# Performance work log

Hardware: AMD Instinct MI355X
Metric: run time of the kernel (lower is better)

## Reference

```python
import jax, jax.numpy as jnp
import numpy as np

R, DIL = 3, 2  # radius, dilation for neighbor correlation


def conv2d(x, w, b):
    # standard 3x3 stride-1 SAME conv, NCHW / OIHW
    y = jax.lax.conv_general_dilated(x, w, (1, 1), 'SAME',
                                     dimension_numbers=('NCHW', 'OIHW', 'NCHW'))
    return y + b[None, :, None, None]


def bilinear_gather(x, py, px):
    # x: (n,c,h,w); py/px: (n,K,h,w) float sampling coords; zero outside bounds
    n, c, h, w = x.shape
    y0 = jnp.floor(py); x0 = jnp.floor(px)
    wy = py - y0; wx = px - x0
    xf = x.reshape(n, c, h * w)

    def gather(yi, xi):
        valid = ((yi >= 0) & (yi < h) & (xi >= 0) & (xi < w)).astype(x.dtype)
        yc = jnp.clip(yi, 0, h - 1).astype(jnp.int32)
        xc = jnp.clip(xi, 0, w - 1).astype(jnp.int32)
        idx = (yc * w + xc).reshape(n, -1)  # (n, K*h*w)
        v = jax.vmap(lambda f, i: f[:, i])(xf, idx)  # (n, c, K*h*w)
        return v.reshape(n, c, *yi.shape[1:]) * valid[:, None]

    v00 = gather(y0, x0); v01 = gather(y0, x0 + 1)
    v10 = gather(y0 + 1, x0); v11 = gather(y0 + 1, x0 + 1)
    wy_ = wy[:, None]; wx_ = wx[:, None]
    return (v00 * (1 - wy_) * (1 - wx_) + v01 * (1 - wy_) * wx_
            + v10 * wy_ * (1 - wx_) + v11 * wy_ * wx_)


def dcn(x, w, b, ow, ob):
    # DCNv2-style modulated deformable 3x3 conv, stride 1, pad 1, 1 deformable group.
    # Offset/mask predicted by an internal conv: channels = [dy(9), dx(9), mask(9)].
    n, c, h, w_ = x.shape
    K = 9
    om = conv2d(x, ow, ob)  # (n, 27, h, w)
    dy, dx = om[:, :K], om[:, K:2 * K]
    mask = jax.nn.sigmoid(om[:, 2 * K:])
    ky, kx = jnp.meshgrid(jnp.arange(-1, 2), jnp.arange(-1, 2), indexing='ij')
    ky = ky.reshape(K).astype(x.dtype); kx = kx.reshape(K).astype(x.dtype)
    yy = jnp.arange(h, dtype=x.dtype)[None, None, :, None]
    xx = jnp.arange(w_, dtype=x.dtype)[None, None, None, :]
    py = yy + ky[None, :, None, None] + dy  # (n,K,h,w)
    px = xx + kx[None, :, None, None] + dx
    samp = bilinear_gather(x, py, px) * mask[:, None]  # (n,c,K,h,w)
    return jnp.einsum('nckhw,ock->nohw', samp, w.reshape(w.shape[0], c, K)) + b[None, :, None, None]


def ncf(f1, f2, radius, dilation):
    # neighbor_correlation_filter: unfold-based sliding-window dot-product attention
    n, c, h, w = f2.shape
    k = 2 * radius + 1
    pad = (k - 1) * dilation // 2
    f2p = jnp.pad(f2, ((0, 0), (0, 0), (pad, pad), (pad, pad)))
    # (n,c,K,h,w), tap order (ky outer, kx inner) matching F.unfold row-major layout
    patches = jnp.stack([f2p[:, :, i * dilation:i * dilation + h, j * dilation:j * dilation + w]
                         for i in range(k) for j in range(k)], axis=2)
    corr = jnp.einsum('nchw,nckhw->nkhw', f1, patches) / jnp.sqrt(jnp.asarray(c, f1.dtype))
    attn = jax.nn.softmax(corr, axis=1)
    sample = jnp.einsum('nkhw,nckhw->nchw', attn, patches)
    return sample, corr


def stargru(x, t, zw, zb, zow, zob, hw, hb, how, hob):
    tx = jnp.concatenate([x, t], axis=1)
    z = jax.nn.sigmoid(dcn(tx, zw, zb, zow, zob))
    r, _ = ncf(t, x, R, DIL)
    xt = jnp.tanh(dcn(jnp.concatenate([r, t], axis=1), hw, hb, how, hob))
    return (1.0 - z) * t + z * xt


def setup_inputs():
    key = jax.random.key(0)
    N, CIN, CH, H, W = 2, 256, 64, 96, 96
    ks = iter(jax.random.split(key, 32))

    def rn(shape, s=0.05):
        return jax.random.normal(next(ks), shape, jnp.float32) * s

    inp = {
        'x': jax.random.normal(next(ks), (N, CIN, H, W), jnp.float32),
        'template': jax.random.normal(next(ks), (N, CH, H, W), jnp.float32),
        'w_in': rn((CH, CIN, 3, 3)), 'b_in': jnp.zeros((CH,), jnp.float32),
        'w_out': rn((CIN, CH, 3, 3)), 'b_out': jnp.zeros((CIN,), jnp.float32),
    }
    for pre in ('enh_z', 'enh_h', 'upd_z', 'upd_h'):
        inp[pre + '_w'] = rn((CH, 2 * CH, 3, 3))
        inp[pre + '_b'] = jnp.zeros((CH,), jnp.float32)
        inp[pre + '_ow'] = rn((27, 2 * CH, 3, 3), 0.01)  # offset/mask conv (small init)
        inp[pre + '_ob'] = jnp.zeros((27,), jnp.float32)
    return inp


def reference(x, template, w_in, b_in, w_out, b_out,
              enh_z_w, enh_z_b, enh_z_ow, enh_z_ob,
              enh_h_w, enh_h_b, enh_h_ow, enh_h_ob,
              upd_z_w, upd_z_b, upd_z_ow, upd_z_ob,
              upd_h_w, upd_h_b, upd_h_ow, upd_h_ob):
    # CrossUpdate forward, post-first-frame branch (self.template is not None)
    xh = conv2d(x, w_in, b_in)
    x_enh = stargru(template, xh,
                    enh_z_w, enh_z_b, enh_z_ow, enh_z_ob,
                    enh_h_w, enh_h_b, enh_h_ow, enh_h_ob)
    new_template = stargru(xh, template,
                           upd_z_w, upd_z_b, upd_z_ow, upd_z_ob,
                           upd_h_w, upd_h_b, upd_h_ow, upd_h_ob)
    out = conv2d(x_enh, w_out, b_out)
    return (out, new_template)
```

## Files before the change

kernel.cpp:

```cpp
#include <hip/hip_runtime.h>
#include <hip/hip_bf16.h>

typedef __hip_bfloat16 bf16;
typedef unsigned short u16;
typedef unsigned int u32;
typedef __attribute__((ext_vector_type(8))) short short8;
typedef __attribute__((ext_vector_type(4))) short bh4;
typedef __attribute__((ext_vector_type(4))) float floatx4;

constexpr int N_ = 2, H_ = 96, W_ = 96, HW_ = H_ * W_;
constexpr int CIN_ = 256, CH_ = 64, C2_ = 128;

__device__ __forceinline__ float sigm(float v) { return 1.0f / (1.0f + __expf(-v)); }
__device__ __forceinline__ short f2b(float v) { bf16 h = __float2bfloat16(v); return *reinterpret_cast<short*>(&h); }
__device__ __forceinline__ float b2f(short s) {
    union { u32 i; float f; } v; v.i = ((u32)(u16)s) << 16; return v.f;
}

constexpr int A_IN_OFF = 0,                         A_IN_SZ  = 64 * 2304;
constexpr int A_OUT_OFF = A_IN_OFF + A_IN_SZ,       A_OUT_SZ = 256 * 576;
constexpr int A_OFF_OFF = A_OUT_OFF + A_OUT_SZ,     A_OFF_SZ = 64 * 1152;
constexpr int A_DCN_OFF = A_OFF_OFF + 4 * A_OFF_SZ, A_DCN_SZ = 64 * 1152;
constexpr int A_TOT = A_DCN_OFF + 4 * A_DCN_SZ;

__global__ __launch_bounds__(256) void cvt_weights(
        const float* __restrict__ w_in, const float* __restrict__ w_out,
        const float* __restrict__ ow0, const float* __restrict__ ow1,
        const float* __restrict__ ow2, const float* __restrict__ ow3,
        const float* __restrict__ w0, const float* __restrict__ w1,
        const float* __restrict__ w2, const float* __restrict__ w3,
        u16* __restrict__ dst) {
    int id = blockIdx.x * 256 + threadIdx.x;
    if (id >= A_TOT) return;
    float v;
    if (id < A_OUT_OFF) {
        int l = id; int m = l / 2304, k = l % 2304; int tap = k >> 8, ic = k & 255;
        v = w_in[m * 2304 + ic * 9 + tap];
    } else if (id < A_OFF_OFF) {
        int l = id - A_OUT_OFF; int m = l / 576, k = l % 576; int tap = k / 64, ic = k & 63;
        v = w_out[m * 576 + ic * 9 + tap];
    } else if (id < A_DCN_OFF) {
        int l = id - A_OFF_OFF; int i = l / A_OFF_SZ, l2 = l % A_OFF_SZ;
        int m = l2 / 1152, k = l2 % 1152; int tap = k >> 7, ic = k & 127;
        const float* s = (i == 0) ? ow0 : (i == 1) ? ow1 : (i == 2) ? ow2 : ow3;
        v = (m < 27) ? s[m * 1152 + ic * 9 + tap] : 0.f;
    } else {
        int l = id - A_DCN_OFF; int i = l / A_DCN_SZ, l2 = l % A_DCN_SZ;
        int m = l2 / 1152, k = l2 % 1152; int tap = k >> 7, c = k & 127;
        const float* s = (i == 0) ? w0 : (i == 1) ? w1 : (i == 2) ? w2 : w3;
        v = s[m * 1152 + c * 9 + tap];
    }
    short sb = f2b(v);
    dst[id] = *reinterpret_cast<u16*>(&sb);
}

__global__ __launch_bounds__(256) void to_nhwc(const float* __restrict__ src, u16* __restrict__ dst, int C) {
    int id = blockIdx.x * 256 + threadIdx.x;
    int c8n = C >> 3;
    if (id >= N_ * HW_ * c8n) return;
    int c8 = id % c8n;
    int pix = id / c8n;
    int n = pix / HW_, p = pix % HW_;
    const float* s = src + ((size_t)n * C + c8 * 8) * HW_ + p;
    short8 vv;
#pragma unroll
    for (int j = 0; j < 8; ++j) vv[j] = f2b(s[(size_t)j * HW_]);
    *reinterpret_cast<short8*>(dst + (size_t)pix * C + c8 * 8) = vv;
}

__global__ __launch_bounds__(256) void concat_dual(const float* __restrict__ tpl, const float* __restrict__ xh,
                                                   u16* __restrict__ ta, u16* __restrict__ tb) {
    int id = blockIdx.x * 256 + threadIdx.x;
    if (id >= N_ * HW_ * 16) return;
    int c8 = id & 15;
    int pix = id >> 4;
    int n = pix / HW_, p = pix % HW_;
    int c = c8 * 8;
    const float* s = (c < 64) ? tpl + ((size_t)n * 64 + c) * HW_ + p
                              : xh + ((size_t)n * 64 + (c - 64)) * HW_ + p;
    short8 vv;
#pragma unroll
    for (int j = 0; j < 8; ++j) vv[j] = f2b(s[(size_t)j * HW_]);
    *reinterpret_cast<short8*>(ta + (size_t)pix * 128 + c) = vv;
    *reinterpret_cast<short8*>(tb + (size_t)pix * 128 + ((c + 64) & 127)) = vv;
}

template <int IC, int OCST>
__device__ __forceinline__ void conv_core(const u16* __restrict__ X,
                                          const u16* __restrict__ A,
                                          const float* __restrict__ bias,
                                          float* __restrict__ out,
                                          int r, int mt, int t) {
    constexpr int K = IC * 9;
    constexpr int ICC = IC / 64;
    __shared__ __align__(16) u16 Xl[3][50][72];
    int n = r / 192;
    int rr = r % 192;
    int y = rr >> 1, px0 = (rr & 1) * 48;
    int w = t >> 6, lane = t & 63, lm = lane & 15, q = lane >> 4;
    const u16* Arow = A + (size_t)(mt * 64 + w * 16 + lm) * K + q * 8;
    floatx4 acc[3];
#pragma unroll
    for (int a = 0; a < 3; ++a) acc[a] = {0.f, 0.f, 0.f, 0.f};
    const short8 zz = {0, 0, 0, 0, 0, 0, 0, 0};

    for (int icc = 0; icc < ICC; ++icc) {
        short8 af[9][2];
#pragma unroll
        for (int tap = 0; tap < 9; ++tap)
#pragma unroll
            for (int ks = 0; ks < 2; ++ks)
                af[tap][ks] = *reinterpret_cast<const short8*>(Arow + tap * IC + icc * 64 + ks * 32);
        __syncthreads();
#pragma unroll
        for (int it = 0; it < 5; ++it) {
            int id = it * 256 + t;
            if (id < 1200) {
                int ch8 = id & 7;
                int tmp = id >> 3;
                int pxl = tmp % 50, row = tmp / 50;
                int xg = px0 - 1 + pxl;
                int yg = y - 1 + row;
                bool vld = (yg >= 0) && (yg < 96) && (xg >= 0) && (xg < 96);
                short8 vv = zz;
                if (vld)
                    vv = *reinterpret_cast<const short8*>(
                        X + ((size_t)(n * HW_ + yg * 96 + xg)) * IC + icc * 64 + ch8 * 8);
                *reinterpret_cast<short8*>(&Xl[row][pxl][ch8 * 8]) = vv;
            }
        }
        __syncthreads();
#pragma unroll
        for (int tap = 0; tap < 9; ++tap) {
            int ky = tap / 3, kx = tap % 3;
#pragma unroll
            for (int ks = 0; ks < 2; ++ks) {
#pragma unroll
                for (int nf = 0; nf < 3; ++nf) {
                    short8 bv = *reinterpret_cast<const short8*>(&Xl[ky][nf * 16 + lm + kx][ks * 32 + q * 8]);
                    acc[nf] = __builtin_amdgcn_mfma_f32_16x16x32_bf16(af[tap][ks], bv, acc[nf], 0, 0, 0);
                }
            }
        }
    }
    int ocb = mt * 64 + w * 16 + q * 4;
#pragma unroll
    for (int nf = 0; nf < 3; ++nf) {
        int px = px0 + nf * 16 + lm;
#pragma unroll
        for (int rr2 = 0; rr2 < 4; ++rr2) {
            int oc = ocb + rr2;
            if (oc < OCST)
                out[((size_t)(n * OCST + oc)) * HW_ + y * 96 + px] = acc[nf][rr2] + bias[oc];
        }
    }
}

template <int IC, int OCST>
__global__ __launch_bounds__(256) void conv_gemm(const u16* __restrict__ X,
                                                 const u16* __restrict__ A,
                                                 const float* __restrict__ bias,
                                                 float* __restrict__ out) {
    conv_core<IC, OCST>(X, A, bias, out, blockIdx.x % 384, blockIdx.x / 384, threadIdx.x);
}

__global__ __launch_bounds__(256) void conv_gemm2(const u16* __restrict__ X0, const u16* __restrict__ X1,
                                                  const u16* __restrict__ A0, const u16* __restrict__ A1,
                                                  const float* __restrict__ b0, const float* __restrict__ b1,
                                                  float* __restrict__ o0, float* __restrict__ o1) {
    int inst = blockIdx.x / 384, r = blockIdx.x % 384;
    conv_core<C2_, 27>(inst ? X1 : X0, inst ? A1 : A0, inst ? b1 : b0, inst ? o1 : o0, r, 0, threadIdx.x);
}

__device__ __forceinline__ void dcn_core(const u16* __restrict__ txh,
                                         const float* __restrict__ om,
                                         const u16* __restrict__ A,
                                         const float* __restrict__ bias,
                                         float* __restrict__ out,
                                         int r, int t) {
    __shared__ __align__(16) u16 Bl[48][72];
    __shared__ float s_wy[432], s_wx[432], s_m[432];
    __shared__ int s_y0[432], s_x0[432];
    int n = r / 192;
    int rr = r % 192;
    int y = rr >> 1, px0 = (rr & 1) * 48;
    for (int e = t; e < 432; e += 256) {
        int k9 = e / 48, xl = e % 48;
        int x = px0 + xl;
        const float* ob = om + (size_t)n * 27 * HW_ + y * 96 + x;
        float dy = ob[(size_t)k9 * HW_];
        float dx = ob[(size_t)(9 + k9) * HW_];
        float ml = ob[(size_t)(18 + k9) * HW_];
        float py = (float)y + (float)(k9 / 3 - 1) + dy;
        float px = (float)x + (float)(k9 % 3 - 1) + dx;
        float fy = floorf(py), fx = floorf(px);
        s_y0[e] = (int)fy; s_x0[e] = (int)fx;
        s_wy[e] = py - fy; s_wx[e] = px - fx; s_m[e] = sigm(ml);
    }
    int w = t >> 6, lane = t & 63, lm = lane & 15, q = lane >> 4;
    const u16* Arow = A + (size_t)(w * 16 + lm) * 1152 + q * 8;
    floatx4 acc[3];
#pragma unroll
    for (int a = 0; a < 3; ++a) acc[a] = {0.f, 0.f, 0.f, 0.f};
    const u16* txn = txh + (size_t)n * HW_ * 128;
    const short8 zz = {0, 0, 0, 0, 0, 0, 0, 0};

    for (int kc = 0; kc < 18; ++kc) {
        int tap = kc >> 1, c0 = (kc & 1) * 64;
        short8 af[2];
#pragma unroll
        for (int ks = 0; ks < 2; ++ks)
            af[ks] = *reinterpret_cast<const short8*>(Arow + kc * 64 + ks * 32);
        __syncthreads();
#pragma unroll
        for (int i = 0; i < 2; ++i) {
            int id = i * 256 + t;
            if (id < 384) {
                int px = id >> 3, ch8 = id & 7;
                int ce = tap * 48 + px;
                int y0 = s_y0[ce], x0 = s_x0[ce];
                float wy = s_wy[ce], wx = s_wx[ce], m = s_m[ce];
                float w00 = (1.f - wy) * (1.f - wx) * m;
                float w01 = (1.f - wy) * wx * m;
                float w10 = wy * (1.f - wx) * m;
                float w11 = wy * wx * m;
                bool yv0 = (y0 >= 0) & (y0 < 96), yv1 = (y0 >= -1) & (y0 < 95);
                bool xv0 = (x0 >= 0) & (x0 < 96), xv1 = (x0 >= -1) & (x0 < 95);
                const u16* base = txn + (long)(y0 * 96 + x0) * 128 + c0 + ch8 * 8;
                short8 v00 = (yv0 && xv0) ? *reinterpret_cast<const short8*>(base) : zz;
                short8 v01 = (yv0 && xv1) ? *reinterpret_cast<const short8*>(base + 128) : zz;
                short8 v10 = (yv1 && xv0) ? *reinterpret_cast<const short8*>(base + 96 * 128) : zz;
                short8 v11 = (yv1 && xv1) ? *reinterpret_cast<const short8*>(base + 96 * 128 + 128) : zz;
                short8 vv;
#pragma unroll
                for (int j = 0; j < 8; ++j) {
                    float f = b2f(v00[j]) * w00 + b2f(v01[j]) * w01 +
                              b2f(v10[j]) * w10 + b2f(v11[j]) * w11;
                    vv[j] = f2b(f);
                }
                *reinterpret_cast<short8*>(&Bl[px][ch8 * 8]) = vv;
            }
        }
        __syncthreads();
#pragma unroll
        for (int ks = 0; ks < 2; ++ks)
#pragma unroll
            for (int nf = 0; nf < 3; ++nf) {
                short8 bv = *reinterpret_cast<const short8*>(&Bl[nf * 16 + lm][ks * 32 + q * 8]);
                acc[nf] = __builtin_amdgcn_mfma_f32_16x16x32_bf16(af[ks], bv, acc[nf], 0, 0, 0);
            }
    }
    int ocb = w * 16 + q * 4;
#pragma unroll
    for (int nf = 0; nf < 3; ++nf) {
        int px = px0 + nf * 16 + lm;
#pragma unroll
        for (int rr2 = 0; rr2 < 4; ++rr2) {
            int oc = ocb + rr2;
            out[((size_t)(n * CH_ + oc)) * HW_ + y * 96 + px] = acc[nf][rr2] + bias[oc];
        }
    }
}

__global__ __launch_bounds__(256) void dcn_gemm2(const u16* __restrict__ X0, const u16* __restrict__ X1,
                                                 const float* __restrict__ om0, const float* __restrict__ om1,
                                                 const u16* __restrict__ A0, const u16* __restrict__ A1,
                                                 const float* __restrict__ b0, const float* __restrict__ b1,
                                                 float* __restrict__ o0, float* __restrict__ o1) {
    int inst = blockIdx.x / 384, r = blockIdx.x % 384;
    dcn_core(inst ? X1 : X0, inst ? om1 : om0, inst ? A1 : A0, inst ? b1 : b0, inst ? o1 : o0, r, threadIdx.x);
}

__global__ __launch_bounds__(256, 4) void ncf2(const u16* __restrict__ in0, const u16* __restrict__ in1,
                                               u16* __restrict__ out0, u16* __restrict__ out1) {
    __shared__ float sc[16][52];
    int t = threadIdx.x;
    int inst = blockIdx.x / 1152, bb = blockIdx.x % 1152;
    const u16* txh = inst ? in1 : in0;
    u16* txh2 = inst ? out1 : out0;
    int lp = t >> 4, j = t & 15;
    int gpx = bb * 16 + lp;
    int n = gpx / HW_, p = gpx % HW_;
    int y = p / 96, x = p % 96;
    const u16* base = txh + (size_t)n * HW_ * 128;
    const u16* f1p = base + (size_t)p * 128 + 64;

    float f1f[64];
#pragma unroll
    for (int c8 = 0; c8 < 8; ++c8) {
        short8 a = *reinterpret_cast<const short8*>(f1p + c8 * 8);
#pragma unroll
        for (int u = 0; u < 8; ++u) f1f[c8 * 8 + u] = b2f(a[u]);
    }
    for (int k = j; k < 49; k += 16) {
        int yy = y + (k / 7) * 2 - 6, xx = x + (k % 7) * 2 - 6;
        float s = 0.f;
        if (yy >= 0 && yy < 96 && xx >= 0 && xx < 96) {
            const u16* f2p = base + (size_t)(yy * 96 + xx) * 128;
#pragma unroll
            for (int c8 = 0; c8 < 8; ++c8) {
                short8 b = *reinterpret_cast<const short8*>(f2p + c8 * 8);
#pragma unroll
                for (int u = 0; u < 8; ++u) s += f1f[c8 * 8 + u] * b2f(b[u]);
            }
        }
        sc[lp][k] = s * 0.125f;
    }
    float mx = -1e30f;
    for (int k = j; k < 49; k += 16) mx = fmaxf(mx, sc[lp][k]);
#pragma unroll
    for (int m = 1; m <= 8; m <<= 1) mx = fmaxf(mx, __shfl_xor(mx, m, 64));
    float e[4];
    float sum = 0.f;
    int cnt = 0;
    for (int k = j; k < 49; k += 16) { e[cnt] = __expf(sc[lp][k] - mx); sum += e[cnt]; ++cnt; }
#pragma unroll
    for (int m = 1; m <= 8; m <<= 1) sum += __shfl_xor(sum, m, 64);
    float inv = 1.f / sum;
    cnt = 0;
    for (int k = j; k < 49; k += 16) sc[lp][k] = e[cnt++] * inv;
    __syncthreads();
    int ch0 = j * 4;
    float acc[4];
#pragma unroll
    for (int u = 0; u < 4; ++u) acc[u] = 0.f;
#pragma unroll
    for (int k = 0; k < 49; ++k) {
        int yy = y + (k / 7) * 2 - 6, xx = x + (k % 7) * 2 - 6;
        if (yy >= 0 && yy < 96 && xx >= 0 && xx < 96) {
            float a = sc[lp][k];
            bh4 f2 = *reinterpret_cast<const bh4*>(base + (size_t)(yy * 96 + xx) * 128 + ch0);
#pragma unroll
            for (int u = 0; u < 4; ++u) acc[u] += a * b2f(f2[u]);
        }
    }
    u16* obase = txh2 + (size_t)n * HW_ * 128 + (size_t)p * 128;
    bh4 ro;
#pragma unroll
    for (int u = 0; u < 4; ++u) ro[u] = f2b(acc[u]);
    *reinterpret_cast<bh4*>(obase + ch0) = ro;
    *reinterpret_cast<bh4*>(obase + 64 + ch0) =
        *reinterpret_cast<const bh4*>(f1p + ch0);
}

__global__ __launch_bounds__(256) void gate_dual(const float* __restrict__ dz_a, const float* __restrict__ dh_a,
                                                 const float* __restrict__ t_a, u16* __restrict__ dst_a,
                                                 const float* __restrict__ dz_b, const float* __restrict__ dh_b,
                                                 const float* __restrict__ t_b, float* __restrict__ dst_b) {
    int inst = blockIdx.x / 576, bb = blockIdx.x % 576;
    int id = bb * 256 + threadIdx.x;
    int c8 = id & 7;
    int pix = id >> 3;
    int n = pix / HW_, p = pix % HW_;
    const float* zpre = inst ? dz_b : dz_a;
    const float* hpre = inst ? dh_b : dh_a;
    const float* tt = inst ? t_b : t_a;
    if (!inst) {
        short8 vv;
#pragma unroll
        for (int j = 0; j < 8; ++j) {
            size_t idx = ((size_t)n * CH_ + c8 * 8 + j) * HW_ + p;
            float z = sigm(zpre[idx]);
            float xt = tanhf(hpre[idx]);
            vv[j] = f2b((1.f - z) * tt[idx] + z * xt);
        }
        *reinterpret_cast<short8*>(dst_a + (size_t)pix * CH_ + c8 * 8) = vv;
    } else {
#pragma unroll
        for (int j = 0; j < 8; ++j) {
            size_t idx = ((size_t)n * CH_ + c8 * 8 + j) * HW_ + p;
            float z = sigm(zpre[idx]);
            float xt = tanhf(hpre[idx]);
            dst_b[idx] = (1.f - z) * tt[idx] + z * xt;
        }
    }
}

extern "C" void kernel_launch(void* const* d_in, const int* in_sizes, int n_in,
                              void* d_out, int out_size, void* d_ws, size_t ws_size,
                              hipStream_t stream) {
    const float* x     = (const float*)d_in[0];
    const float* tpl   = (const float*)d_in[1];
    const float* w_in  = (const float*)d_in[2];
    const float* b_in  = (const float*)d_in[3];
    const float* w_out = (const float*)d_in[4];
    const float* b_out = (const float*)d_in[5];
    const float *pw[4], *pb[4], *pow_[4], *pob[4];
    for (int i = 0; i < 4; ++i) {
        pw[i]   = (const float*)d_in[6 + 4 * i];
        pb[i]   = (const float*)d_in[7 + 4 * i];
        pow_[i] = (const float*)d_in[8 + 4 * i];
        pob[i]  = (const float*)d_in[9 + 4 * i];
    }
    float* out_main = (float*)d_out;
    float* out_ntpl = out_main + (size_t)N_ * CIN_ * HW_;

    u16* Aws = (u16*)d_ws;
    u16* xT     = Aws + A_TOT;
    u16* txh_a  = xT + (size_t)N_ * HW_ * CIN_;
    u16* txh_b  = txh_a + (size_t)N_ * HW_ * C2_;
    u16* txh2_a = txh_b + (size_t)N_ * HW_ * C2_;
    u16* txh2_b = txh2_a + (size_t)N_ * HW_ * C2_;
    u16* xeh    = txh2_b + (size_t)N_ * HW_ * C2_;
    float* fws = (float*)(xeh + (size_t)N_ * HW_ * CH_);
    size_t off = 0;
    float* xh   = fws + off; off += (size_t)N_ * CH_ * HW_;
    float* om_a = fws + off; off += (size_t)N_ * 27 * HW_;
    float* om_b = fws + off; off += (size_t)N_ * 27 * HW_;
    float* dz_a = fws + off; off += (size_t)N_ * CH_ * HW_;
    float* dz_b = fws + off; off += (size_t)N_ * CH_ * HW_;
    float* dh_a = fws + off; off += (size_t)N_ * CH_ * HW_;
    float* dh_b = fws + off; off += (size_t)N_ * CH_ * HW_;

    cvt_weights<<<(A_TOT + 255) / 256, 256, 0, stream>>>(
        w_in, w_out, pow_[0], pow_[1], pow_[2], pow_[3], pw[0], pw[1], pw[2], pw[3], Aws);
    to_nhwc<<<2304, 256, 0, stream>>>(x, xT, CIN_);
    conv_gemm<CIN_, 64><<<384, 256, 0, stream>>>(xT, Aws + A_IN_OFF, b_in, xh);

    concat_dual<<<1152, 256, 0, stream>>>(tpl, xh, txh_a, txh_b);
    conv_gemm2<<<768, 256, 0, stream>>>(txh_a, txh_b,
        Aws + A_OFF_OFF + 0 * A_OFF_SZ, Aws + A_OFF_OFF + 2 * A_OFF_SZ, pob[0], pob[2], om_a, om_b);
    dcn_gemm2<<<768, 256, 0, stream>>>(txh_a, txh_b, om_a, om_b,
        Aws + A_DCN_OFF + 0 * A_DCN_SZ, Aws + A_DCN_OFF + 2 * A_DCN_SZ, pb[0], pb[2], dz_a, dz_b);
    ncf2<<<2304, 256, 0, stream>>>(txh_a, txh_b, txh2_a, txh2_b);
    conv_gemm2<<<768, 256, 0, stream>>>(txh2_a, txh2_b,
        Aws + A_OFF_OFF + 1 * A_OFF_SZ, Aws + A_OFF_OFF + 3 * A_OFF_SZ, pob[1], pob[3], om_a, om_b);
    dcn_gemm2<<<768, 256, 0, stream>>>(txh2_a, txh2_b, om_a, om_b,
        Aws + A_DCN_OFF + 1 * A_DCN_SZ, Aws + A_DCN_OFF + 3 * A_DCN_SZ, pb[1], pb[3], dh_a, dh_b);
    gate_dual<<<1152, 256, 0, stream>>>(dz_a, dh_a, xh, xeh, dz_b, dh_b, tpl, out_ntpl);

    conv_gemm<CH_, 256><<<1536, 256, 0, stream>>>(xeh, Aws + A_OUT_OFF, b_out, out_main);
}
```

Baseline: 364.3 us.

## Stage NCF neighbor window and query features in shared memory

```diff
diff --git a/kernel.cpp b/kernel.cpp
--- a/kernel.cpp
+++ b/kernel.cpp
@@ -273,36 +273,48 @@
 
 __global__ __launch_bounds__(256, 4) void ncf2(const u16* __restrict__ in0, const u16* __restrict__ in1,
                                                u16* __restrict__ out0, u16* __restrict__ out1) {
+    __shared__ __align__(16) u16 sF2[7][28][72];
+    __shared__ __align__(16) u16 sF1[16][72];
     __shared__ float sc[16][52];
     int t = threadIdx.x;
     int inst = blockIdx.x / 1152, bb = blockIdx.x % 1152;
     const u16* txh = inst ? in1 : in0;
     u16* txh2 = inst ? out1 : out0;
+    int n = bb / 576, rem = bb % 576;
+    int y = rem / 6, x0 = (rem % 6) * 16;
+    const u16* base = txh + (size_t)n * HW_ * 128;
+    const short8 zz = {0, 0, 0, 0, 0, 0, 0, 0};
+
+    for (int id = t; id < 1568; id += 256) {
+        int ch8 = id & 7;
+        int tmp = id >> 3;
+        int px = tmp % 28, row = tmp / 28;
+        int yy = y + row * 2 - 6;
+        int xg = x0 - 6 + px;
+        short8 vv = zz;
+        if (yy >= 0 && yy < 96 && xg >= 0 && xg < 96)
+            vv = *reinterpret_cast<const short8*>(base + (size_t)(yy * 96 + xg) * 128 + ch8 * 8);
+        *reinterpret_cast<short8*>(&sF2[row][px][ch8 * 8]) = vv;
+    }
+    if (t < 128) {
+        int ch8 = t & 7, lp0 = t >> 3;
+        short8 vv = *reinterpret_cast<const short8*>(base + (size_t)(y * 96 + x0 + lp0) * 128 + 64 + ch8 * 8);
+        *reinterpret_cast<short8*>(&sF1[lp0][ch8 * 8]) = vv;
+    }
+    __syncthreads();
+
     int lp = t >> 4, j = t & 15;
-    int gpx = bb * 16 + lp;
-    int n = gpx / HW_, p = gpx % HW_;
-    int y = p / 96, x = p % 96;
-    const u16* base = txh + (size_t)n * HW_ * 128;
-    const u16* f1p = base + (size_t)p * 128 + 64;
-
-    float f1f[64];
-#pragma unroll
-    for (int c8 = 0; c8 < 8; ++c8) {
-        short8 a = *reinterpret_cast<const short8*>(f1p + c8 * 8);
-#pragma unroll
-        for (int u = 0; u < 8; ++u) f1f[c8 * 8 + u] = b2f(a[u]);
-    }
     for (int k = j; k < 49; k += 16) {
-        int yy = y + (k / 7) * 2 - 6, xx = x + (k % 7) * 2 - 6;
+        int ky = k / 7, kx = k % 7;
+        const u16* f2p = &sF2[ky][lp + 2 * kx][0];
+        const u16* f1p = &sF1[lp][0];
         float s = 0.f;
-        if (yy >= 0 && yy < 96 && xx >= 0 && xx < 96) {
-            const u16* f2p = base + (size_t)(yy * 96 + xx) * 128;
-#pragma unroll
-            for (int c8 = 0; c8 < 8; ++c8) {
-                short8 b = *reinterpret_cast<const short8*>(f2p + c8 * 8);
-#pragma unroll
-                for (int u = 0; u < 8; ++u) s += f1f[c8 * 8 + u] * b2f(b[u]);
-            }
+#pragma unroll
+        for (int c8 = 0; c8 < 8; ++c8) {
+            short8 a = *reinterpret_cast<const short8*>(f1p + c8 * 8);
+            short8 b = *reinterpret_cast<const short8*>(f2p + c8 * 8);
+#pragma unroll
+            for (int u = 0; u < 8; ++u) s += b2f(a[u]) * b2f(b[u]);
         }
         sc[lp][k] = s * 0.125f;
     }
@@ -326,21 +338,20 @@
     for (int u = 0; u < 4; ++u) acc[u] = 0.f;
 #pragma unroll
     for (int k = 0; k < 49; ++k) {
-        int yy = y + (k / 7) * 2 - 6, xx = x + (k % 7) * 2 - 6;
-        if (yy >= 0 && yy < 96 && xx >= 0 && xx < 96) {
-            float a = sc[lp][k];
-            bh4 f2 = *reinterpret_cast<const bh4*>(base + (size_t)(yy * 96 + xx) * 128 + ch0);
-#pragma unroll
-            for (int u = 0; u < 4; ++u) acc[u] += a * b2f(f2[u]);
-        }
-    }
+        int ky = k / 7, kx = k % 7;
+        float a = sc[lp][k];
+        bh4 f2 = *reinterpret_cast<const bh4*>(&sF2[ky][lp + 2 * kx][ch0]);
+#pragma unroll
+        for (int u = 0; u < 4; ++u) acc[u] += a * b2f(f2[u]);
+    }
+    int p = y * 96 + x0 + lp;
     u16* obase = txh2 + (size_t)n * HW_ * 128 + (size_t)p * 128;
     bh4 ro;
 #pragma unroll
     for (int u = 0; u < 4; ++u) ro[u] = f2b(acc[u]);
     *reinterpret_cast<bh4*>(obase + ch0) = ro;
     *reinterpret_cast<bh4*>(obase + 64 + ch0) =
-        *reinterpret_cast<const bh4*>(f1p + ch0);
+        *reinterpret_cast<const bh4*>(&sF1[lp][ch0]);
 }
 
 __global__ __launch_bounds__(256) void gate_dual(const float* __restrict__ dz_a, const float* __restrict__ dh_a,
```

Result: faster. 344.0 us (-5.6%).
